# Kernel tuning notes

Hardware: AMD Instinct MI355X
Metric: run time of the kernel (lower is better)

Reference implementation:

```python
import jax, jax.numpy as jnp
import numpy as np

VOCAB = 100000
EMBED = 300
BATCH = 131072
NEG = 10


def setup_inputs() -> dict:
    key = jax.random.key(0)
    k1, k2, k3, k4, k5 = jax.random.split(key, 5)
    center_words = jax.random.randint(k1, (BATCH,), 0, VOCAB)
    context_words = jax.random.randint(k2, (BATCH,), 0, VOCAB)
    neg_samples = jax.random.randint(k3, (BATCH, NEG), 0, VOCAB)
    in_embed = jax.random.normal(k4, (VOCAB, EMBED), dtype=jnp.float32)
    out_embed = jax.random.normal(k5, (VOCAB, EMBED), dtype=jnp.float32)
    return {
        "center_words": center_words,
        "context_words": context_words,
        "neg_samples": neg_samples,
        "in_embed": in_embed,
        "out_embed": out_embed,
    }


def reference(center_words, context_words, neg_samples, in_embed, out_embed):
    center_e = in_embed[center_words]          # [B, D]
    context_e = out_embed[context_words]       # [B, D]
    neg_e = out_embed[neg_samples]             # [B, K, D]
    pos_scores = jnp.sum(center_e * context_e, axis=1)            # [B]
    neg_scores = jnp.einsum("bkd,bd->bk", neg_e, center_e)        # [B, K]
    pos_loss = jax.nn.log_sigmoid(pos_scores)                      # [B]
    neg_loss = jnp.sum(jax.nn.log_sigmoid(-neg_scores), axis=1)   # [B]
    return -jnp.mean(pos_loss + neg_loss)
```

## Files before the change

### kernel.cpp

```cpp
#include <hip/hip_runtime.h>
#include <math.h>

#define VOCABN 100000
#define EMBED 300
#define BATCH 131072
#define NEG 10
#define RQ 19
#define PD 5

typedef float float2v __attribute__((ext_vector_type(2)));


template <bool HI>
__device__ __forceinline__ float2v cvt2(unsigned int w) {
    return __builtin_amdgcn_cvt_pk_f32_fp8((int)w, HI);
}
template <bool HI>
__device__ __forceinline__ unsigned int pk2(unsigned int old, float a, float b) {
    return (unsigned int)__builtin_amdgcn_cvt_pk_fp8_f32(a, b, (int)old, HI);
}

__device__ __forceinline__ float dqf(const float* c, uint4 q) {
    float2v p;
    float s = 0.0f;
    p = cvt2<false>(q.x); s += c[0]  * p.x + c[1]  * p.y;
    p = cvt2<true >(q.x); s += c[2]  * p.x + c[3]  * p.y;
    p = cvt2<false>(q.y); s += c[4]  * p.x + c[5]  * p.y;
    p = cvt2<true >(q.y); s += c[6]  * p.x + c[7]  * p.y;
    p = cvt2<false>(q.z); s += c[8]  * p.x + c[9]  * p.y;
    p = cvt2<true >(q.z); s += c[10] * p.x + c[11] * p.y;
    p = cvt2<false>(q.w); s += c[12] * p.x + c[13] * p.y;
    p = cvt2<true >(q.w); s += c[14] * p.x + c[15] * p.y;
    return s;
}

__device__ __forceinline__ void unp16(uint4 q, float* f) {
    float2v p;
    p = cvt2<false>(q.x); f[0]  = p.x; f[1]  = p.y;
    p = cvt2<true >(q.x); f[2]  = p.x; f[3]  = p.y;
    p = cvt2<false>(q.y); f[4]  = p.x; f[5]  = p.y;
    p = cvt2<true >(q.y); f[6]  = p.x; f[7]  = p.y;
    p = cvt2<false>(q.z); f[8]  = p.x; f[9]  = p.y;
    p = cvt2<true >(q.z); f[10] = p.x; f[11] = p.y;
    p = cvt2<false>(q.w); f[12] = p.x; f[13] = p.y;
    p = cvt2<true >(q.w); f[14] = p.x; f[15] = p.y;
}


__device__ __forceinline__ float dot4(const float4 a, const float4 b) {
    return a.x * b.x + a.y * b.y + a.z * b.z + a.w * b.w;
}

__device__ __forceinline__ float lsig(float x) {
    float ax = fabsf(x);
    return fminf(x, 0.0f) - __logf(1.0f + __expf(-ax));
}

__device__ __forceinline__ float reduce16(float v) {
    v += __shfl_xor(v, 1);
    v += __shfl_xor(v, 2);
    v += __shfl_xor(v, 4);
    v += __shfl_xor(v, 8);
    return v;
}

__global__ void sgns_zero_acc(double* acc) { *acc = 0.0; }

__global__ void sgns_finalize(const double* __restrict__ acc, float* __restrict__ out) {
    *out = (float)(-(*acc) / (double)BATCH);
}


__global__ __launch_bounds__(256) void cvt_fp8(const float* __restrict__ src,
                                               uint4* __restrict__ dst, int nrows) {
    const int total = nrows * RQ;
    const int stride = gridDim.x * blockDim.x;
    for (int i = blockIdx.x * blockDim.x + threadIdx.x; i < total; i += stride) {
        int r = i / RQ;
        int q = i - r * RQ;
        const float4* s = reinterpret_cast<const float4*>(src + (size_t)r * EMBED + q * 16);
        float4 a = s[0], b = s[1], c = s[2];
        float4 d = make_float4(0.f, 0.f, 0.f, 0.f);
        if (q != RQ - 1) d = s[3];
        uint4 o;
        unsigned int w;
        w = pk2<false>(0, a.x, a.y); o.x = pk2<true>(w, a.z, a.w);
        w = pk2<false>(0, b.x, b.y); o.y = pk2<true>(w, b.z, b.w);
        w = pk2<false>(0, c.x, c.y); o.z = pk2<true>(w, c.z, c.w);
        w = pk2<false>(0, d.x, d.y); o.w = pk2<true>(w, d.z, d.w);
        dst[i] = o;
    }
}


__global__ __launch_bounds__(256) void sgns_fp8(
    const int* __restrict__ center_words,
    const int* __restrict__ context_words,
    const int* __restrict__ neg_samples,
    const uint4* __restrict__ inQ,
    const uint4* __restrict__ outQ,
    double* __restrict__ acc)
{
    const int lane = threadIdx.x & 15;
    const int group = (blockIdx.x * blockDim.x + threadIdx.x) >> 4;
    const int nGroups = (gridDim.x * blockDim.x) >> 4;
    const int tl = (lane < 3) ? lane : 0;
    const float tmask = (lane < 3) ? 1.0f : 0.0f;

    float tsum = 0.0f;

    for (int b = group; b < BATCH; b += nGroups) {
        const int cw = center_words[b];
        const int xw = context_words[b];
        const int2* np = reinterpret_cast<const int2*>(neg_samples + (size_t)b * NEG);
        int2 q0 = np[0], q1 = np[1], q2 = np[2], q3 = np[3], q4 = np[4];
        int idx[11] = {xw, q0.x, q0.y, q1.x, q1.y, q2.x, q2.y, q3.x, q3.y, q4.x, q4.y};

        const uint4* cp = inQ + (size_t)cw * RQ;
        uint4 cm = cp[lane];
        uint4 ct = cp[16 + tl];
        float cf[32];
        unp16(cm, cf);
        unp16(ct, cf + 16);
        #pragma unroll
        for (int j = 16; j < 32; ++j) cf[j] *= tmask;

        float part[11];
        uint4 bm[PD], bt[PD];
        #pragma unroll
        for (int j = 0; j < PD - 1; ++j) {
            const uint4* p = outQ + (size_t)idx[j] * RQ;
            bm[j] = p[lane]; bt[j] = p[16 + tl];
        }
        #pragma unroll
        for (int j = 0; j < 11; ++j) {
            if (j + PD - 1 < 11) {
                const uint4* p = outQ + (size_t)idx[j + PD - 1] * RQ;
                bm[(j + PD - 1) % PD] = p[lane];
                bt[(j + PD - 1) % PD] = p[16 + tl];
            }
            part[j] = dqf(cf, bm[j % PD]) + dqf(cf + 16, bt[j % PD]);
        }

        #pragma unroll
        for (int j = 0; j < 11; ++j) part[j] = reduce16(part[j]);

        float loss = lsig(part[0]);
        #pragma unroll
        for (int j = 1; j < 11; ++j) loss += lsig(-part[j]);

        tsum += (lane == 0) ? loss : 0.0f;
    }

    float w = tsum;
    #pragma unroll
    for (int m = 1; m < 64; m <<= 1) w += __shfl_xor(w, m);

    __shared__ double ssum[4];
    const int wid = threadIdx.x >> 6;
    if ((threadIdx.x & 63) == 0) ssum[wid] = (double)w;
    __syncthreads();
    if (threadIdx.x == 0) {
        atomicAdd(acc, ssum[0] + ssum[1] + ssum[2] + ssum[3]);
    }
}


__global__ __launch_bounds__(256) void sgns_f32(
    const int* __restrict__ center_words,
    const int* __restrict__ context_words,
    const int* __restrict__ neg_samples,
    const float* __restrict__ in_embed,
    const float* __restrict__ out_embed,
    double* __restrict__ acc)
{
    const int lane = threadIdx.x & 15;
    const int group = (blockIdx.x * blockDim.x + threadIdx.x) >> 4;
    const int nGroups = (gridDim.x * blockDim.x) >> 4;

    const float4* inE = reinterpret_cast<const float4*>(in_embed);
    const float4* outE = reinterpret_cast<const float4*>(out_embed);
    const int RU = EMBED / 4;
    const int TAIL = RU - 64;

    float tsum = 0.0f;

    for (int b = group; b < BATCH; b += nGroups) {
        const int c = center_words[b];
        const int ctx = context_words[b];

        const float4* crow = inE + (size_t)c * RU;
        float4 c0 = crow[lane + 0];
        float4 c1 = crow[lane + 16];
        float4 c2 = crow[lane + 32];
        float4 c3 = crow[lane + 48];
        float4 c4 = make_float4(0.f, 0.f, 0.f, 0.f);
        if (lane < TAIL) c4 = crow[lane + 64];

        const float4* xrow = outE + (size_t)ctx * RU;
        float p = dot4(c0, xrow[lane + 0])
                + dot4(c1, xrow[lane + 16])
                + dot4(c2, xrow[lane + 32])
                + dot4(c3, xrow[lane + 48]);
        if (lane < TAIL) p += dot4(c4, xrow[lane + 64]);
        p = reduce16(p);

        float loss = lsig(p);

        #pragma unroll
        for (int k = 0; k < NEG; ++k) {
            const int nk = neg_samples[b * NEG + k];
            const float4* nrow = outE + (size_t)nk * RU;
            float s = dot4(c0, nrow[lane + 0])
                    + dot4(c1, nrow[lane + 16])
                    + dot4(c2, nrow[lane + 32])
                    + dot4(c3, nrow[lane + 48]);
            if (lane < TAIL) s += dot4(c4, nrow[lane + 64]);
            s = reduce16(s);
            loss += lsig(-s);
        }

        tsum += (lane == 0) ? loss : 0.0f;
    }

    float w = tsum;
    #pragma unroll
    for (int m = 1; m < 64; m <<= 1) w += __shfl_xor(w, m);

    __shared__ double ssum[4];
    const int wid = threadIdx.x >> 6;
    if ((threadIdx.x & 63) == 0) ssum[wid] = (double)w;
    __syncthreads();
    if (threadIdx.x == 0) {
        atomicAdd(acc, ssum[0] + ssum[1] + ssum[2] + ssum[3]);
    }
}


extern "C" void kernel_launch(void* const* d_in, const int* in_sizes, int n_in,
                              void* d_out, int out_size, void* d_ws, size_t ws_size,
                              hipStream_t stream) {
    const int* center = (const int*)d_in[0];
    const int* context = (const int*)d_in[1];
    const int* negs = (const int*)d_in[2];
    const float* inE = (const float*)d_in[3];
    const float* outE = (const float*)d_in[4];
    float* out = (float*)d_out;
    double* acc = (double*)d_ws;

    sgns_zero_acc<<<1, 1, 0, stream>>>(acc);

    const size_t TBL_BYTES = (size_t)VOCABN * RQ * 16;
    const size_t need = 256 + 2 * TBL_BYTES;

    if (ws_size >= need) {
        uint4* inQ = (uint4*)((char*)d_ws + 256);
        uint4* outQ = (uint4*)((char*)d_ws + 256 + TBL_BYTES);
        cvt_fp8<<<4096, 256, 0, stream>>>(inE, inQ, VOCABN);
        cvt_fp8<<<4096, 256, 0, stream>>>(outE, outQ, VOCABN);
        sgns_fp8<<<2048, 256, 0, stream>>>(center, context, negs,
                                           (const uint4*)inQ, (const uint4*)outQ, acc);
    } else {
        sgns_f32<<<2048, 256, 0, stream>>>(center, context, negs, inE, outE, acc);
    }

    sgns_finalize<<<1, 1, 0, stream>>>(acc, out);
}
```

Baseline: 151.4 us.

## Split FP8 embedding tables into aligned 256-byte main and 64-byte tail arrays

Each quantized FP8 row is now stored as a 256-byte main block holding 16 uint4s and a separate 64-byte tail block padded to 4 uint4s. Before, rows were packed contiguously at a 304-byte stride. The split keeps gathers cache-line aligned, so each row's main fetch touches fewer lines than a misaligned 304-byte record. The prefetch depth also drops from 5 to 3, lowering register pressure. In exchange the gather loop issues two separate loads to different arrays, the tables take slightly more memory, and the shallower prefetch may hide less latency.

```diff
diff --git a/kernel.cpp b/kernel.cpp
--- a/kernel.cpp
+++ b/kernel.cpp
@@ -5,8 +5,7 @@
 #define EMBED 300
 #define BATCH 131072
 #define NEG 10
-#define RQ 19
-#define PD 5
+#define PD 3
 
 typedef float float2v __attribute__((ext_vector_type(2)));
 
@@ -71,24 +70,40 @@
 }
 
 
-__global__ __launch_bounds__(256) void cvt_fp8(const float* __restrict__ src,
-                                               uint4* __restrict__ dst, int nrows) {
-    const int total = nrows * RQ;
+__global__ __launch_bounds__(256) void cvt_fp8s(const float* __restrict__ src,
+                                                uint4* __restrict__ mainT,
+                                                uint4* __restrict__ tailT, int nrows) {
+    const int total = nrows * 20;
     const int stride = gridDim.x * blockDim.x;
     for (int i = blockIdx.x * blockDim.x + threadIdx.x; i < total; i += stride) {
-        int r = i / RQ;
-        int q = i - r * RQ;
-        const float4* s = reinterpret_cast<const float4*>(src + (size_t)r * EMBED + q * 16);
-        float4 a = s[0], b = s[1], c = s[2];
-        float4 d = make_float4(0.f, 0.f, 0.f, 0.f);
-        if (q != RQ - 1) d = s[3];
-        uint4 o;
-        unsigned int w;
-        w = pk2<false>(0, a.x, a.y); o.x = pk2<true>(w, a.z, a.w);
-        w = pk2<false>(0, b.x, b.y); o.y = pk2<true>(w, b.z, b.w);
-        w = pk2<false>(0, c.x, c.y); o.z = pk2<true>(w, c.z, c.w);
-        w = pk2<false>(0, d.x, d.y); o.w = pk2<true>(w, d.z, d.w);
-        dst[i] = o;
+        const int r = i / 20;
+        const int q = i - r * 20;
+        if (q < 16) {
+            const float4* s = reinterpret_cast<const float4*>(src + (size_t)r * EMBED + q * 16);
+            float4 a = s[0], b = s[1], c = s[2], d = s[3];
+            uint4 o;
+            unsigned int w;
+            w = pk2<false>(0, a.x, a.y); o.x = pk2<true>(w, a.z, a.w);
+            w = pk2<false>(0, b.x, b.y); o.y = pk2<true>(w, b.z, b.w);
+            w = pk2<false>(0, c.x, c.y); o.z = pk2<true>(w, c.z, c.w);
+            w = pk2<false>(0, d.x, d.y); o.w = pk2<true>(w, d.z, d.w);
+            mainT[(size_t)r * 16 + q] = o;
+        } else {
+            const int t = q - 16;
+            uint4 o = make_uint4(0u, 0u, 0u, 0u);
+            if (t < 3) {
+                const float4* s = reinterpret_cast<const float4*>(src + (size_t)r * EMBED + 256 + t * 16);
+                float4 a = s[0], b = s[1], c = s[2];
+                float4 d = make_float4(0.f, 0.f, 0.f, 0.f);
+                if (t < 2) d = s[3];
+                unsigned int w;
+                w = pk2<false>(0, a.x, a.y); o.x = pk2<true>(w, a.z, a.w);
+                w = pk2<false>(0, b.x, b.y); o.y = pk2<true>(w, b.z, b.w);
+                w = pk2<false>(0, c.x, c.y); o.z = pk2<true>(w, c.z, c.w);
+                w = pk2<false>(0, d.x, d.y); o.w = pk2<true>(w, d.z, d.w);
+            }
+            tailT[(size_t)r * 4 + t] = o;
+        }
     }
 }
 
@@ -97,8 +112,8 @@
     const int* __restrict__ center_words,
     const int* __restrict__ context_words,
     const int* __restrict__ neg_samples,
-    const uint4* __restrict__ inQ,
-    const uint4* __restrict__ outQ,
+    const uint4* __restrict__ inM,  const uint4* __restrict__ inT,
+    const uint4* __restrict__ outM, const uint4* __restrict__ outT,
     double* __restrict__ acc)
 {
     const int lane = threadIdx.x & 15;
@@ -116,9 +131,8 @@
         int2 q0 = np[0], q1 = np[1], q2 = np[2], q3 = np[3], q4 = np[4];
         int idx[11] = {xw, q0.x, q0.y, q1.x, q1.y, q2.x, q2.y, q3.x, q3.y, q4.x, q4.y};
 
-        const uint4* cp = inQ + (size_t)cw * RQ;
-        uint4 cm = cp[lane];
-        uint4 ct = cp[16 + tl];
+        uint4 cm = inM[(size_t)cw * 16 + lane];
+        uint4 ct = inT[(size_t)cw * 4 + tl];
         float cf[32];
         unp16(cm, cf);
         unp16(ct, cf + 16);
@@ -129,15 +143,14 @@
         uint4 bm[PD], bt[PD];
         #pragma unroll
         for (int j = 0; j < PD - 1; ++j) {
-            const uint4* p = outQ + (size_t)idx[j] * RQ;
-            bm[j] = p[lane]; bt[j] = p[16 + tl];
+            bm[j] = outM[(size_t)idx[j] * 16 + lane];
+            bt[j] = outT[(size_t)idx[j] * 4 + tl];
         }
         #pragma unroll
         for (int j = 0; j < 11; ++j) {
             if (j + PD - 1 < 11) {
-                const uint4* p = outQ + (size_t)idx[j + PD - 1] * RQ;
-                bm[(j + PD - 1) % PD] = p[lane];
-                bt[(j + PD - 1) % PD] = p[16 + tl];
+                bm[(j + PD - 1) % PD] = outM[(size_t)idx[j + PD - 1] * 16 + lane];
+                bt[(j + PD - 1) % PD] = outT[(size_t)idx[j + PD - 1] * 4 + tl];
             }
             part[j] = dqf(cf, bm[j % PD]) + dqf(cf + 16, bt[j % PD]);
         }
@@ -250,16 +263,20 @@
 
     sgns_zero_acc<<<1, 1, 0, stream>>>(acc);
 
-    const size_t TBL_BYTES = (size_t)VOCABN * RQ * 16;
-    const size_t need = 256 + 2 * TBL_BYTES;
+    const size_t MAIN_B = (size_t)VOCABN * 16 * 16;
+    const size_t TAIL_B = (size_t)VOCABN * 4 * 16;
+    const size_t need = 256 + 2 * (MAIN_B + TAIL_B);
 
     if (ws_size >= need) {
-        uint4* inQ = (uint4*)((char*)d_ws + 256);
-        uint4* outQ = (uint4*)((char*)d_ws + 256 + TBL_BYTES);
-        cvt_fp8<<<4096, 256, 0, stream>>>(inE, inQ, VOCABN);
-        cvt_fp8<<<4096, 256, 0, stream>>>(outE, outQ, VOCABN);
+        char* base = (char*)d_ws + 256;
+        uint4* inM  = (uint4*)(base);
+        uint4* inT  = (uint4*)(base + MAIN_B);
+        uint4* outM = (uint4*)(base + MAIN_B + TAIL_B);
+        uint4* outT = (uint4*)(base + 2 * MAIN_B + TAIL_B);
+        cvt_fp8s<<<4096, 256, 0, stream>>>(inE, inM, inT, VOCABN);
+        cvt_fp8s<<<4096, 256, 0, stream>>>(outE, outM, outT, VOCABN);
         sgns_fp8<<<2048, 256, 0, stream>>>(center, context, negs,
-                                           (const uint4*)inQ, (const uint4*)outQ, acc);
+                                           inM, inT, outM, outT, acc);
     } else {
         sgns_f32<<<2048, 256, 0, stream>>>(center, context, negs, inE, outE, acc);
     }
```

Result: no change. 151.1 us (-0.2%).
